# Kernel tuning notes

Measured on AMD Instinct MI355X. Metric: run time of the kernel, lower is better.

## Reference

```python
import jax, jax.numpy as jnp
import numpy as np

NUM_RELATIONS = 4
N_NODES = 20000
N_EDGES = 320000
F_IN = 128
HID = 128
EMB = 128


def _rgcn_conv(x, src, dst, edge_type, edge_weight, W, root, bias):
    """One WeightedRGCNConv layer.
    x: [N, in]; W: [R, in, out]; root: [in, out]; bias: [out].
    Math identical to m = einsum('ei,eio->eo', x[src], W[edge_type]) but computed
    as R grouped matmuls to avoid materializing the [E, in, out] weight copy.
    """
    xj = x[src]  # [E, in] gather
    m = jnp.zeros((xj.shape[0], W.shape[2]), dtype=x.dtype)
    for r in range(W.shape[0]):  # fixed small relation count
        mask = (edge_type == r).astype(x.dtype)[:, None]
        m = m + mask * (xj @ W[r])
    m = m * edge_weight[:, None]
    out = jax.ops.segment_sum(m, dst, num_segments=x.shape[0])  # scatter_add
    return out + x @ root + bias


def setup_inputs() -> dict:
    key = jax.random.key(0)
    ks = jax.random.split(key, 10)
    return {
        "x": jax.random.normal(ks[0], (N_NODES, F_IN), dtype=jnp.float32),
        "edge_index": jax.random.randint(ks[1], (2, N_EDGES), 0, N_NODES, dtype=jnp.int64 if jax.config.jax_enable_x64 else jnp.int32).astype(jnp.int32),
        "edge_type": jax.random.randint(ks[2], (N_EDGES,), 0, NUM_RELATIONS).astype(jnp.int32),
        "edge_weight": jax.random.uniform(ks[3], (N_EDGES,), dtype=jnp.float32),
        "W1": jax.random.normal(ks[4], (NUM_RELATIONS, F_IN, HID), dtype=jnp.float32) * 0.05,
        "root1": jax.random.normal(ks[5], (F_IN, HID), dtype=jnp.float32) * 0.05,
        "b1": jax.random.normal(ks[6], (HID,), dtype=jnp.float32) * 0.05,
        "W2": jax.random.normal(ks[7], (NUM_RELATIONS, HID, EMB), dtype=jnp.float32) * 0.05,
        "root2": jax.random.normal(ks[8], (HID, EMB), dtype=jnp.float32) * 0.05,
        "b2": jax.random.normal(ks[9], (EMB,), dtype=jnp.float32) * 0.05,
    }


def reference(x, edge_index, edge_type, edge_weight, W1, root1, b1, W2, root2, b2):
    src, dst = edge_index[0], edge_index[1]
    # min-max normalize edge weights (as in RGCN.forward)
    ew = (edge_weight - edge_weight.min()) / (edge_weight.max() - edge_weight.min() + 1e-08)
    h = jax.nn.relu(_rgcn_conv(x, src, dst, edge_type, ew, W1, root1, b1))
    h = _rgcn_conv(h, src, dst, edge_type, ew, W2, root2, b2)
    return h
```

## Files before the change

### kernel.cpp

```cpp
#include <hip/hip_runtime.h>

#define NN 20000
#define NE 320000
#define FD 128
#define KTOT 640
#define NSTEP 20

typedef float f32x4 __attribute__((ext_vector_type(4)));
typedef __bf16 bf16x4 __attribute__((ext_vector_type(4)));
typedef __bf16 bf16x8 __attribute__((ext_vector_type(8)));

__device__ __forceinline__ unsigned f2ord(float f) {
  unsigned u = __float_as_uint(f);
  return (u & 0x80000000u) ? ~u : (u | 0x80000000u);
}
__device__ __forceinline__ float ord2f(unsigned u) {
  return (u & 0x80000000u) ? __uint_as_float(u & 0x7FFFFFFFu) : __uint_as_float(~u);
}
__device__ __forceinline__ unsigned pkbf(float a, float b) {
  union { __bf16 h[2]; unsigned u; } p;
  p.h[0] = (__bf16)a; p.h[1] = (__bf16)b; return p.u;
}
__device__ __forceinline__ void gld16(const void* src, void* lds) {
  __builtin_amdgcn_global_load_lds(
      (const unsigned int __attribute__((address_space(1)))*)src,
      (unsigned int __attribute__((address_space(3)))*)lds, 16, 0, 0);
}

__global__ void init_kernel(unsigned* mm, int* deg) {
  int i = blockIdx.x * blockDim.x + threadIdx.x;
  if (i == 0) { mm[0] = 0xFFFFFFFFu; mm[1] = 0u; }
  if (i < NN) deg[i] = 0;
}

__global__ void histmm_kernel(const int* __restrict__ dst, const float* __restrict__ ew,
                              int* deg, unsigned* mm) {
  __shared__ unsigned smn[256], smx[256];
  unsigned lmn = 0xFFFFFFFFu, lmx = 0u;
  for (int i = blockIdx.x * blockDim.x + threadIdx.x; i < NE; i += gridDim.x * blockDim.x) {
    atomicAdd(&deg[dst[i]], 1);
    unsigned o = f2ord(ew[i]);
    lmn = (o < lmn) ? o : lmn;
    lmx = (o > lmx) ? o : lmx;
  }
  smn[threadIdx.x] = lmn; smx[threadIdx.x] = lmx;
  __syncthreads();
  for (int s = 128; s > 0; s >>= 1) {
    if (threadIdx.x < s) {
      unsigned a = smn[threadIdx.x], b = smn[threadIdx.x + s];
      smn[threadIdx.x] = (b < a) ? b : a;
      unsigned c = smx[threadIdx.x], d = smx[threadIdx.x + s];
      smx[threadIdx.x] = (d > c) ? d : c;
    }
    __syncthreads();
  }
  if (threadIdx.x == 0) { atomicMin(&mm[0], smn[0]); atomicMax(&mm[1], smx[0]); }
}

__global__ void scan_kernel(const int* __restrict__ deg, int* offs, int* cursor) {
  __shared__ int part[1024];
  const int CH = (NN + 1023) / 1024;
  int t = threadIdx.x;
  int b = t * CH;
  int e = (b + CH < NN) ? (b + CH) : NN;
  int s = 0;
  for (int i = b; i < e; ++i) s += deg[i];
  part[t] = s;
  __syncthreads();
  for (int off = 1; off < 1024; off <<= 1) {
    int v = part[t];
    int add = (t >= off) ? part[t - off] : 0;
    __syncthreads();
    part[t] = v + add;
    __syncthreads();
  }
  int excl = (t == 0) ? 0 : part[t - 1];
  for (int i = b; i < e; ++i) { offs[i] = excl; cursor[i] = excl; excl += deg[i]; }
  if (t == 1023) offs[NN] = part[1023];
}

__global__ void fill_kernel(const int* __restrict__ src, const int* __restrict__ dst,
                            const int* __restrict__ et, const float* __restrict__ ew,
                            const unsigned* __restrict__ mm, int* cursor,
                            int2* __restrict__ ed) {
  int e = blockIdx.x * blockDim.x + threadIdx.x;
  if (e >= NE) return;
  float mn = ord2f(mm[0]), mx = ord2f(mm[1]);
  float inv = 1.0f / (mx - mn + 1e-8f);
  int d = dst[e];
  int pos = atomicAdd(&cursor[d], 1);
  ed[pos] = make_int2(src[e] | (et[e] << 28), __float_as_int((ew[e] - mn) * inv));
}

__global__ void prep_wt_both(const float* __restrict__ W1, const float* __restrict__ r1,
                             const float* __restrict__ W2, const float* __restrict__ r2,
                             __bf16* __restrict__ wt1, __bf16* __restrict__ wt2) {
  int idx = blockIdx.x * blockDim.x + threadIdx.x;
  if (idx >= 2 * FD * KTOT) return;
  int which = idx / (FD * KTOT);
  int rem = idx % (FD * KTOT);
  int n = rem / KTOT, k = rem % KTOT;
  const float* W = which ? W2 : W1;
  const float* rt = which ? r2 : r1;
  __bf16* wt = which ? wt2 : wt1;
  float v = (k < 512) ? W[(size_t)k * FD + n] : rt[(size_t)(k - 512) * FD + n];
  wt[rem] = (__bf16)v;
}

template <int BF16IN>
__global__ __launch_bounds__(256) void aggregate_kernel(
    const float* __restrict__ xf, const unsigned* __restrict__ xb,
    const int* __restrict__ offs, const int2* __restrict__ ed,
    __bf16* __restrict__ g) {
  int node = (int)((blockIdx.x * blockDim.x + threadIdx.x) >> 6);
  int lane = threadIdx.x & 63;
  if (node >= NN) return;
  int beg = offs[node], end = offs[node + 1];
  float a00 = 0.f, a01 = 0.f, a10 = 0.f, a11 = 0.f;
  float a20 = 0.f, a21 = 0.f, a30 = 0.f, a31 = 0.f;

#define LOADP(E, P0, P1)                                                        \
  do {                                                                          \
    int s_ = (E).x & 0x0FFFFFFF;                                                \
    if (BF16IN) {                                                               \
      unsigned u_ = xb[(size_t)s_ * 64 + lane];                                 \
      P0 = __uint_as_float(u_ << 16);                                           \
      P1 = __uint_as_float(u_ & 0xFFFF0000u);                                   \
    } else {                                                                    \
      float2 v_ = *(const float2*)(xf + (size_t)s_ * FD + lane * 2);            \
      P0 = v_.x; P1 = v_.y;                                                     \
    }                                                                           \
  } while (0)
#define ACCP(E, P0, P1)                                                         \
  do {                                                                          \
    float w_ = __int_as_float((E).y);                                           \
    unsigned r_ = ((unsigned)(E).x) >> 28;                                      \
    float w0_ = (r_ == 0) ? w_ : 0.f, w1_ = (r_ == 1) ? w_ : 0.f;               \
    float w2_ = (r_ == 2) ? w_ : 0.f, w3_ = (r_ == 3) ? w_ : 0.f;               \
    a00 += w0_ * (P0); a01 += w0_ * (P1);                                       \
    a10 += w1_ * (P0); a11 += w1_ * (P1);                                       \
    a20 += w2_ * (P0); a21 += w2_ * (P1);                                       \
    a30 += w3_ * (P0); a31 += w3_ * (P1);                                       \
  } while (0)

  int j = beg;
  for (; j + 4 <= end; j += 4) {
    int2 e0 = ed[j], e1 = ed[j + 1], e2 = ed[j + 2], e3 = ed[j + 3];
    float p00, p01, p10, p11, p20, p21, p30, p31;
    LOADP(e0, p00, p01); LOADP(e1, p10, p11);
    LOADP(e2, p20, p21); LOADP(e3, p30, p31);
    ACCP(e0, p00, p01); ACCP(e1, p10, p11);
    ACCP(e2, p20, p21); ACCP(e3, p30, p31);
  }
  for (; j < end; ++j) {
    int2 e = ed[j];
    float p0, p1;
    LOADP(e, p0, p1);
    ACCP(e, p0, p1);
  }
#undef LOADP
#undef ACCP

  unsigned* g32 = (unsigned*)(g + (size_t)node * KTOT);
  g32[0 * 64 + lane] = pkbf(a00, a01);
  g32[1 * 64 + lane] = pkbf(a10, a11);
  g32[2 * 64 + lane] = pkbf(a20, a21);
  g32[3 * 64 + lane] = pkbf(a30, a31);
  if (BF16IN) {
    g32[4 * 64 + lane] = xb[(size_t)node * 64 + lane];
  } else {
    float2 v = *(const float2*)(xf + (size_t)node * FD + lane * 2);
    g32[4 * 64 + lane] = pkbf(v.x, v.y);
  }
}

template <int OUT_BF16>
__global__ __launch_bounds__(512) void gemm_kernel(
    const __bf16* __restrict__ gA, const __bf16* __restrict__ wt,
    const float* __restrict__ bias, float* __restrict__ outf,
    __bf16* __restrict__ outb) {
  __shared__ __bf16 As[2][64 * 32];
  __shared__ __bf16 Bs[2][128 * 32];
  int tid = threadIdx.x;
  int wave = tid >> 6, lane = tid & 63;
  int wr = wave >> 1, wc = wave & 1;
  int m0 = blockIdx.x * 64;
  int rl = wr * 16 + (lane & 15);
  int kfe = (lane >> 4) * 8;

  unsigned rowpack = 0, colpack[4];
  {
    int arow = tid >> 3, akof = (tid & 7) * 4;
    int bn = tid >> 2, bkof = (tid & 3) * 8;
    bf16x4 v4, one4;
    bf16x8 v8, one8;
#pragma unroll
    for (int i = 0; i < 4; ++i) one4[i] = (__bf16)1.0f;
#pragma unroll
    for (int i = 0; i < 8; ++i) one8[i] = (__bf16)1.0f;
    __bf16 rv = (__bf16)((float)arow * 0.015625f);
#pragma unroll
    for (int i = 0; i < 4; ++i) v4[i] = rv;
    *(bf16x4*)(&As[0][arow * 32 + akof]) = v4;
    *(bf16x8*)(&Bs[0][bn * 32 + bkof]) = one8;
    __syncthreads();
    bf16x8 pa = *(const bf16x8*)(&As[0][rl * 32 + kfe]);
    bf16x8 pb = *(const bf16x8*)(&Bs[0][(wc * 64 + (lane & 15)) * 32 + kfe]);
    f32x4 P1 = __builtin_amdgcn_mfma_f32_16x16x32_bf16(pa, pb, (f32x4){0.f, 0.f, 0.f, 0.f}, 0, 0, 0);
    __syncthreads();
    __bf16 cv = (__bf16)((float)bn * 0.0078125f);
#pragma unroll
    for (int i = 0; i < 8; ++i) v8[i] = cv;
    *(bf16x4*)(&As[0][arow * 32 + akof]) = one4;
    *(bf16x8*)(&Bs[0][bn * 32 + bkof]) = v8;
    __syncthreads();
    bf16x8 pa1 = *(const bf16x8*)(&As[0][rl * 32 + kfe]);
#pragma unroll
    for (int j = 0; j < 4; ++j)
      rowpack |= ((unsigned)(int)(P1[j] * 2.0f + 0.5f)) << (8 * j);
#pragma unroll
    for (int fn = 0; fn < 4; ++fn) {
      bf16x8 pbc = *(const bf16x8*)(&Bs[0][(wc * 64 + fn * 16 + (lane & 15)) * 32 + kfe]);
      f32x4 P2 = __builtin_amdgcn_mfma_f32_16x16x32_bf16(pa1, pbc, (f32x4){0.f, 0.f, 0.f, 0.f}, 0, 0, 0);
      unsigned cp = 0;
#pragma unroll
      for (int j = 0; j < 4; ++j)
        cp |= ((unsigned)(int)(P2[j] * 4.0f + 0.5f)) << (8 * j);
      colpack[fn] = cp;
    }
    __syncthreads();
  }

  f32x4 acc[4];
#pragma unroll
  for (int i = 0; i < 4; ++i) acc[i] = (f32x4){0.f, 0.f, 0.f, 0.f};

  auto stage = [&](int buf, int k0) {
    if (tid < 256) {
      int row = tid >> 2;
      int m = m0 + row;
      if (m >= NN) m = NN - 1;
      gld16(gA + (size_t)m * KTOT + k0 + (tid & 3) * 8, &As[buf][(tid >> 6) * 512]);
    } else {
      int t = tid - 256;
      int wv = t >> 6;
      int r0 = t >> 2;
      gld16(wt + (size_t)r0 * KTOT + k0 + (t & 3) * 8, &Bs[buf][wv * 512]);
      gld16(wt + (size_t)(64 + r0) * KTOT + k0 + (t & 3) * 8, &Bs[buf][2048 + wv * 512]);
    }
  };

  stage(0, 0);
  __syncthreads();
  int cur = 0;
  for (int step = 0; step < NSTEP; ++step) {
    if (step + 1 < NSTEP) stage(cur ^ 1, (step + 1) * 32);
    bf16x8 a = *(const bf16x8*)(&As[cur][rl * 32 + kfe]);
#pragma unroll
    for (int fn = 0; fn < 4; ++fn) {
      bf16x8 b = *(const bf16x8*)(&Bs[cur][(wc * 64 + fn * 16 + (lane & 15)) * 32 + kfe]);
      acc[fn] = __builtin_amdgcn_mfma_f32_16x16x32_bf16(a, b, acc[fn], 0, 0, 0);
    }
    __syncthreads();
    cur ^= 1;
  }

#pragma unroll
  for (int fn = 0; fn < 4; ++fn) {
#pragma unroll
    for (int j = 0; j < 4; ++j) {
      int rloc = (int)((rowpack >> (8 * j)) & 255u);
      int col = (int)((colpack[fn] >> (8 * j)) & 255u);
      int m = m0 + rloc;
      if (m < NN) {
        float v = acc[fn][j] + bias[col];
        if (OUT_BF16) {
          v = fmaxf(v, 0.f);
          outb[(size_t)m * FD + col] = (__bf16)v;
        } else {
          outf[(size_t)m * FD + col] = v;
        }
      }
    }
  }
}

extern "C" void kernel_launch(void* const* d_in, const int* in_sizes, int n_in,
                              void* d_out, int out_size, void* d_ws, size_t ws_size,
                              hipStream_t stream) {
  const float* x  = (const float*)d_in[0];
  const int*   ei = (const int*)d_in[1];
  const int*   et = (const int*)d_in[2];
  const float* ew = (const float*)d_in[3];
  const float* W1 = (const float*)d_in[4];
  const float* r1 = (const float*)d_in[5];
  const float* b1 = (const float*)d_in[6];
  const float* W2 = (const float*)d_in[7];
  const float* r2 = (const float*)d_in[8];
  const float* b2 = (const float*)d_in[9];
  float* out = (float*)d_out;
  const int* src = ei;
  const int* dst = ei + NE;

  char* w = (char*)d_ws;
  size_t o = 0;
  auto take = [&](size_t bytes) -> char* {
    char* p = w + o;
    o += (bytes + 255) & ~(size_t)255;
    return p;
  };
  unsigned* mm  = (unsigned*)take(8);
  int* deg      = (int*)take((size_t)NN * 4);
  int* offs     = (int*)take((size_t)(NN + 1) * 4);
  int* cursor   = (int*)take((size_t)NN * 4);
  int2* ed      = (int2*)take((size_t)NE * 8);
  __bf16* g     = (__bf16*)take((size_t)NN * KTOT * 2);
  __bf16* h1    = (__bf16*)take((size_t)NN * FD * 2);
  __bf16* wt1   = (__bf16*)take((size_t)FD * KTOT * 2);
  __bf16* wt2   = (__bf16*)take((size_t)FD * KTOT * 2);
  (void)ws_size; (void)n_in; (void)in_sizes; (void)out_size;

  hipLaunchKernelGGL(init_kernel, dim3((NN + 255) / 256), dim3(256), 0, stream, mm, deg);
  hipLaunchKernelGGL(histmm_kernel, dim3(512), dim3(256), 0, stream, dst, ew, deg, mm);
  hipLaunchKernelGGL(scan_kernel, dim3(1), dim3(1024), 0, stream, deg, offs, cursor);
  hipLaunchKernelGGL(fill_kernel, dim3((NE + 255) / 256), dim3(256), 0, stream,
                     src, dst, et, ew, mm, cursor, ed);
  hipLaunchKernelGGL(prep_wt_both, dim3((2 * FD * KTOT + 255) / 256), dim3(256), 0, stream,
                     W1, r1, W2, r2, wt1, wt2);
  hipLaunchKernelGGL((aggregate_kernel<0>), dim3(NN / 4), dim3(256), 0, stream,
                     x, (const unsigned*)nullptr, offs, ed, g);
  hipLaunchKernelGGL((gemm_kernel<1>), dim3((NN + 63) / 64), dim3(512), 0, stream,
                     g, wt1, b1, (float*)nullptr, h1);
  hipLaunchKernelGGL((aggregate_kernel<1>), dim3(NN / 4), dim3(256), 0, stream,
                     (const float*)nullptr, (const unsigned*)h1, offs, ed, g);
  hipLaunchKernelGGL((gemm_kernel<0>), dim3((NN + 63) / 64), dim3(512), 0, stream,
                     g, wt2, b2, out, (__bf16*)nullptr);
}
```

Before: 168.7 us.

## Fuse edge aggregation with GEMM per node tile through LDS

Replaces the separate aggregate and GEMM kernels with one fused kernel per layer. Each block aggregates 32 nodes into a swizzled LDS tile and then multiplies that tile by the bf16 weights, with B fragments read straight from global memory. This removes the round trip of the 640-wide g buffer through global memory and two kernel launches. Layer-1 input x is now converted to bf16 up front in init_kernel, which lowers the precision of the first gather. The cost is less parallelism for the gather, since each wave serially handles 4 nodes, and no LDS staging or reuse of the weights.

```diff
diff --git a/kernel.cpp b/kernel.cpp
--- a/kernel.cpp
+++ b/kernel.cpp
@@ -4,10 +4,9 @@
 #define NE 320000
 #define FD 128
 #define KTOT 640
-#define NSTEP 20
+#define BM 32
 
 typedef float f32x4 __attribute__((ext_vector_type(4)));
-typedef __bf16 bf16x4 __attribute__((ext_vector_type(4)));
 typedef __bf16 bf16x8 __attribute__((ext_vector_type(8)));
 
 __device__ __forceinline__ unsigned f2ord(float f) {
@@ -21,16 +20,19 @@
   union { __bf16 h[2]; unsigned u; } p;
   p.h[0] = (__bf16)a; p.h[1] = (__bf16)b; return p.u;
 }
-__device__ __forceinline__ void gld16(const void* src, void* lds) {
-  __builtin_amdgcn_global_load_lds(
-      (const unsigned int __attribute__((address_space(1)))*)src,
-      (unsigned int __attribute__((address_space(3)))*)lds, 16, 0, 0);
-}
-
-__global__ void init_kernel(unsigned* mm, int* deg) {
+
+__global__ void init_kernel(unsigned* mm, int* deg,
+                            const float* __restrict__ x, unsigned* __restrict__ xb) {
   int i = blockIdx.x * blockDim.x + threadIdx.x;
   if (i == 0) { mm[0] = 0xFFFFFFFFu; mm[1] = 0u; }
   if (i < NN) deg[i] = 0;
+  if (i < NN * FD / 4) {
+    float4 v = *(const float4*)(x + (size_t)i * 4);
+    uint2 p;
+    p.x = pkbf(v.x, v.y);
+    p.y = pkbf(v.z, v.w);
+    *(uint2*)(xb + (size_t)i * 2) = p;
+  }
 }
 
 __global__ void histmm_kernel(const int* __restrict__ dst, const float* __restrict__ ew,
@@ -107,180 +109,137 @@
   wt[rem] = (__bf16)v;
 }
 
-template <int BF16IN>
-__global__ __launch_bounds__(256) void aggregate_kernel(
-    const float* __restrict__ xf, const unsigned* __restrict__ xb,
+template <int BF16OUT>
+__global__ __launch_bounds__(512, 2) void fused_kernel(
+    const unsigned* __restrict__ xb,
     const int* __restrict__ offs, const int2* __restrict__ ed,
-    __bf16* __restrict__ g) {
-  int node = (int)((blockIdx.x * blockDim.x + threadIdx.x) >> 6);
-  int lane = threadIdx.x & 63;
-  if (node >= NN) return;
-  int beg = offs[node], end = offs[node + 1];
-  float a00 = 0.f, a01 = 0.f, a10 = 0.f, a11 = 0.f;
-  float a20 = 0.f, a21 = 0.f, a30 = 0.f, a31 = 0.f;
-
-#define LOADP(E, P0, P1)                                                        \
-  do {                                                                          \
-    int s_ = (E).x & 0x0FFFFFFF;                                                \
-    if (BF16IN) {                                                               \
-      unsigned u_ = xb[(size_t)s_ * 64 + lane];                                 \
-      P0 = __uint_as_float(u_ << 16);                                           \
-      P1 = __uint_as_float(u_ & 0xFFFF0000u);                                   \
-    } else {                                                                    \
-      float2 v_ = *(const float2*)(xf + (size_t)s_ * FD + lane * 2);            \
-      P0 = v_.x; P1 = v_.y;                                                     \
-    }                                                                           \
+    const __bf16* __restrict__ wt, const float* __restrict__ bias,
+    float* __restrict__ outf, __bf16* __restrict__ outb) {
+  __shared__ unsigned As32[BM * 320];
+  int tid = threadIdx.x;
+  int wave = tid >> 6, lane = tid & 63;
+  int wr = wave >> 2, wc = wave & 3;
+  int m0 = blockIdx.x * BM;
+  int rl = wr * 16 + (lane & 15);
+  int kfe = (lane >> 4) * 8;
+  int c0 = wc * 32 + (lane & 15);
+  const f32x4 zz = {0.f, 0.f, 0.f, 0.f};
+
+  unsigned rowpack = 0, colpack0 = 0, colpack1 = 0;
+  {
+    if (tid < 256) {
+      int row = tid >> 3;
+      int wl = (tid & 7) * 2;
+      unsigned val = pkbf((float)row * 0.03125f, (float)row * 0.03125f);
+      int sw2 = (row & 7) << 2;
+      As32[row * 320 + (wl ^ sw2)] = val;
+      As32[row * 320 + ((wl + 1) ^ sw2)] = val;
+    }
+    __syncthreads();
+    const char* Arow = (const char*)As32 + rl * 1280;
+    int swb = (rl & 7) << 4;
+    bf16x8 pa = *(const bf16x8*)(Arow + ((kfe * 2) ^ swb));
+    bf16x8 ones, bp0, bp1;
+#pragma unroll
+    for (int i = 0; i < 8; ++i) ones[i] = (__bf16)1.0f;
+    __bf16 c0v = (__bf16)((float)c0 * 0.0078125f);
+    __bf16 c1v = (__bf16)((float)(c0 + 16) * 0.0078125f);
+#pragma unroll
+    for (int i = 0; i < 8; ++i) { bp0[i] = c0v; bp1[i] = c1v; }
+    f32x4 P1 = __builtin_amdgcn_mfma_f32_16x16x32_bf16(pa, ones, zz, 0, 0, 0);
+    f32x4 P2a = __builtin_amdgcn_mfma_f32_16x16x32_bf16(ones, bp0, zz, 0, 0, 0);
+    f32x4 P2b = __builtin_amdgcn_mfma_f32_16x16x32_bf16(ones, bp1, zz, 0, 0, 0);
+#pragma unroll
+    for (int j = 0; j < 4; ++j) {
+      rowpack |= ((unsigned)(int)(P1[j] + 0.5f)) << (8 * j);
+      colpack0 |= ((unsigned)(int)(P2a[j] * 4.0f + 0.5f)) << (8 * j);
+      colpack1 |= ((unsigned)(int)(P2b[j] * 4.0f + 0.5f)) << (8 * j);
+    }
+    __syncthreads();
+  }
+
+#define LOADP(E, P0, P1)                                                \
+  do {                                                                  \
+    int s_ = (E).x & 0x0FFFFFFF;                                        \
+    unsigned u_ = xb[(size_t)s_ * 64 + lane];                           \
+    P0 = __uint_as_float(u_ << 16);                                     \
+    P1 = __uint_as_float(u_ & 0xFFFF0000u);                             \
   } while (0)
-#define ACCP(E, P0, P1)                                                         \
-  do {                                                                          \
-    float w_ = __int_as_float((E).y);                                           \
-    unsigned r_ = ((unsigned)(E).x) >> 28;                                      \
-    float w0_ = (r_ == 0) ? w_ : 0.f, w1_ = (r_ == 1) ? w_ : 0.f;               \
-    float w2_ = (r_ == 2) ? w_ : 0.f, w3_ = (r_ == 3) ? w_ : 0.f;               \
-    a00 += w0_ * (P0); a01 += w0_ * (P1);                                       \
-    a10 += w1_ * (P0); a11 += w1_ * (P1);                                       \
-    a20 += w2_ * (P0); a21 += w2_ * (P1);                                       \
-    a30 += w3_ * (P0); a31 += w3_ * (P1);                                       \
+#define ACCP(E, P0, P1)                                                 \
+  do {                                                                  \
+    float w_ = __int_as_float((E).y);                                   \
+    unsigned r_ = ((unsigned)(E).x) >> 28;                              \
+    float w0_ = (r_ == 0) ? w_ : 0.f, w1_ = (r_ == 1) ? w_ : 0.f;       \
+    float w2_ = (r_ == 2) ? w_ : 0.f, w3_ = (r_ == 3) ? w_ : 0.f;       \
+    a00 += w0_ * (P0); a01 += w0_ * (P1);                               \
+    a10 += w1_ * (P0); a11 += w1_ * (P1);                               \
+    a20 += w2_ * (P0); a21 += w2_ * (P1);                               \
+    a30 += w3_ * (P0); a31 += w3_ * (P1);                               \
   } while (0)
 
-  int j = beg;
-  for (; j + 4 <= end; j += 4) {
-    int2 e0 = ed[j], e1 = ed[j + 1], e2 = ed[j + 2], e3 = ed[j + 3];
-    float p00, p01, p10, p11, p20, p21, p30, p31;
-    LOADP(e0, p00, p01); LOADP(e1, p10, p11);
-    LOADP(e2, p20, p21); LOADP(e3, p30, p31);
-    ACCP(e0, p00, p01); ACCP(e1, p10, p11);
-    ACCP(e2, p20, p21); ACCP(e3, p30, p31);
-  }
-  for (; j < end; ++j) {
-    int2 e = ed[j];
-    float p0, p1;
-    LOADP(e, p0, p1);
-    ACCP(e, p0, p1);
+  for (int nl = 0; nl < 4; ++nl) {
+    int nloc = (wave << 2) + nl;
+    int node = m0 + nloc;
+    int beg = offs[node], end = offs[node + 1];
+    float a00 = 0.f, a01 = 0.f, a10 = 0.f, a11 = 0.f;
+    float a20 = 0.f, a21 = 0.f, a30 = 0.f, a31 = 0.f;
+    int j = beg;
+    for (; j + 4 <= end; j += 4) {
+      int2 e0 = ed[j], e1 = ed[j + 1], e2 = ed[j + 2], e3 = ed[j + 3];
+      float p00, p01, p10, p11, p20, p21, p30, p31;
+      LOADP(e0, p00, p01); LOADP(e1, p10, p11);
+      LOADP(e2, p20, p21); LOADP(e3, p30, p31);
+      ACCP(e0, p00, p01); ACCP(e1, p10, p11);
+      ACCP(e2, p20, p21); ACCP(e3, p30, p31);
+    }
+    for (; j < end; ++j) {
+      int2 e = ed[j];
+      float p0, p1;
+      LOADP(e, p0, p1);
+      ACCP(e, p0, p1);
+    }
+    int sw2 = (nloc & 7) << 2;
+    unsigned* row = As32 + nloc * 320;
+    row[(0 * 64 + lane) ^ sw2] = pkbf(a00, a01);
+    row[(1 * 64 + lane) ^ sw2] = pkbf(a10, a11);
+    row[(2 * 64 + lane) ^ sw2] = pkbf(a20, a21);
+    row[(3 * 64 + lane) ^ sw2] = pkbf(a30, a31);
+    row[(4 * 64 + lane) ^ sw2] = xb[(size_t)node * 64 + lane];
   }
 #undef LOADP
 #undef ACCP
-
-  unsigned* g32 = (unsigned*)(g + (size_t)node * KTOT);
-  g32[0 * 64 + lane] = pkbf(a00, a01);
-  g32[1 * 64 + lane] = pkbf(a10, a11);
-  g32[2 * 64 + lane] = pkbf(a20, a21);
-  g32[3 * 64 + lane] = pkbf(a30, a31);
-  if (BF16IN) {
-    g32[4 * 64 + lane] = xb[(size_t)node * 64 + lane];
-  } else {
-    float2 v = *(const float2*)(xf + (size_t)node * FD + lane * 2);
-    g32[4 * 64 + lane] = pkbf(v.x, v.y);
-  }
-}
-
-template <int OUT_BF16>
-__global__ __launch_bounds__(512) void gemm_kernel(
-    const __bf16* __restrict__ gA, const __bf16* __restrict__ wt,
-    const float* __restrict__ bias, float* __restrict__ outf,
-    __bf16* __restrict__ outb) {
-  __shared__ __bf16 As[2][64 * 32];
-  __shared__ __bf16 Bs[2][128 * 32];
-  int tid = threadIdx.x;
-  int wave = tid >> 6, lane = tid & 63;
-  int wr = wave >> 1, wc = wave & 1;
-  int m0 = blockIdx.x * 64;
-  int rl = wr * 16 + (lane & 15);
-  int kfe = (lane >> 4) * 8;
-
-  unsigned rowpack = 0, colpack[4];
-  {
-    int arow = tid >> 3, akof = (tid & 7) * 4;
-    int bn = tid >> 2, bkof = (tid & 3) * 8;
-    bf16x4 v4, one4;
-    bf16x8 v8, one8;
-#pragma unroll
-    for (int i = 0; i < 4; ++i) one4[i] = (__bf16)1.0f;
-#pragma unroll
-    for (int i = 0; i < 8; ++i) one8[i] = (__bf16)1.0f;
-    __bf16 rv = (__bf16)((float)arow * 0.015625f);
-#pragma unroll
-    for (int i = 0; i < 4; ++i) v4[i] = rv;
-    *(bf16x4*)(&As[0][arow * 32 + akof]) = v4;
-    *(bf16x8*)(&Bs[0][bn * 32 + bkof]) = one8;
-    __syncthreads();
-    bf16x8 pa = *(const bf16x8*)(&As[0][rl * 32 + kfe]);
-    bf16x8 pb = *(const bf16x8*)(&Bs[0][(wc * 64 + (lane & 15)) * 32 + kfe]);
-    f32x4 P1 = __builtin_amdgcn_mfma_f32_16x16x32_bf16(pa, pb, (f32x4){0.f, 0.f, 0.f, 0.f}, 0, 0, 0);
-    __syncthreads();
-    __bf16 cv = (__bf16)((float)bn * 0.0078125f);
-#pragma unroll
-    for (int i = 0; i < 8; ++i) v8[i] = cv;
-    *(bf16x4*)(&As[0][arow * 32 + akof]) = one4;
-    *(bf16x8*)(&Bs[0][bn * 32 + bkof]) = v8;
-    __syncthreads();
-    bf16x8 pa1 = *(const bf16x8*)(&As[0][rl * 32 + kfe]);
-#pragma unroll
-    for (int j = 0; j < 4; ++j)
-      rowpack |= ((unsigned)(int)(P1[j] * 2.0f + 0.5f)) << (8 * j);
-#pragma unroll
-    for (int fn = 0; fn < 4; ++fn) {
-      bf16x8 pbc = *(const bf16x8*)(&Bs[0][(wc * 64 + fn * 16 + (lane & 15)) * 32 + kfe]);
-      f32x4 P2 = __builtin_amdgcn_mfma_f32_16x16x32_bf16(pa1, pbc, (f32x4){0.f, 0.f, 0.f, 0.f}, 0, 0, 0);
-      unsigned cp = 0;
-#pragma unroll
-      for (int j = 0; j < 4; ++j)
-        cp |= ((unsigned)(int)(P2[j] * 4.0f + 0.5f)) << (8 * j);
-      colpack[fn] = cp;
-    }
-    __syncthreads();
-  }
-
-  f32x4 acc[4];
-#pragma unroll
-  for (int i = 0; i < 4; ++i) acc[i] = (f32x4){0.f, 0.f, 0.f, 0.f};
-
-  auto stage = [&](int buf, int k0) {
-    if (tid < 256) {
-      int row = tid >> 2;
-      int m = m0 + row;
-      if (m >= NN) m = NN - 1;
-      gld16(gA + (size_t)m * KTOT + k0 + (tid & 3) * 8, &As[buf][(tid >> 6) * 512]);
-    } else {
-      int t = tid - 256;
-      int wv = t >> 6;
-      int r0 = t >> 2;
-      gld16(wt + (size_t)r0 * KTOT + k0 + (t & 3) * 8, &Bs[buf][wv * 512]);
-      gld16(wt + (size_t)(64 + r0) * KTOT + k0 + (t & 3) * 8, &Bs[buf][2048 + wv * 512]);
-    }
-  };
-
-  stage(0, 0);
   __syncthreads();
-  int cur = 0;
-  for (int step = 0; step < NSTEP; ++step) {
-    if (step + 1 < NSTEP) stage(cur ^ 1, (step + 1) * 32);
-    bf16x8 a = *(const bf16x8*)(&As[cur][rl * 32 + kfe]);
-#pragma unroll
-    for (int fn = 0; fn < 4; ++fn) {
-      bf16x8 b = *(const bf16x8*)(&Bs[cur][(wc * 64 + fn * 16 + (lane & 15)) * 32 + kfe]);
-      acc[fn] = __builtin_amdgcn_mfma_f32_16x16x32_bf16(a, b, acc[fn], 0, 0, 0);
-    }
-    __syncthreads();
-    cur ^= 1;
-  }
-
-#pragma unroll
-  for (int fn = 0; fn < 4; ++fn) {
-#pragma unroll
-    for (int j = 0; j < 4; ++j) {
-      int rloc = (int)((rowpack >> (8 * j)) & 255u);
-      int col = (int)((colpack[fn] >> (8 * j)) & 255u);
-      int m = m0 + rloc;
-      if (m < NN) {
-        float v = acc[fn][j] + bias[col];
-        if (OUT_BF16) {
-          v = fmaxf(v, 0.f);
-          outb[(size_t)m * FD + col] = (__bf16)v;
-        } else {
-          outf[(size_t)m * FD + col] = v;
-        }
-      }
+
+  f32x4 acc0 = zz, acc1 = zz;
+  const __bf16* w0p = wt + (size_t)c0 * KTOT + kfe;
+  const __bf16* w1p = w0p + 16 * KTOT;
+  const char* Arow = (const char*)As32 + rl * 1280;
+  int swb = (rl & 7) << 4;
+#pragma unroll
+  for (int step = 0; step < 20; ++step) {
+    int b = (step * 64 + kfe * 2) ^ swb;
+    bf16x8 a = *(const bf16x8*)(Arow + b);
+    bf16x8 b0 = *(const bf16x8*)(w0p + step * 32);
+    bf16x8 b1 = *(const bf16x8*)(w1p + step * 32);
+    acc0 = __builtin_amdgcn_mfma_f32_16x16x32_bf16(a, b0, acc0, 0, 0, 0);
+    acc1 = __builtin_amdgcn_mfma_f32_16x16x32_bf16(a, b1, acc1, 0, 0, 0);
+  }
+
+#pragma unroll
+  for (int j = 0; j < 4; ++j) {
+    int rloc = (int)((rowpack >> (8 * j)) & 255u);
+    size_t m = (size_t)(m0 + rloc);
+    {
+      int col = (int)((colpack0 >> (8 * j)) & 255u);
+      float v = acc0[j] + bias[col];
+      if (BF16OUT) outb[m * FD + col] = (__bf16)fmaxf(v, 0.f);
+      else outf[m * FD + col] = v;
+    }
+    {
+      int col = (int)((colpack1 >> (8 * j)) & 255u);
+      float v = acc1[j] + bias[col];
+      if (BF16OUT) outb[m * FD + col] = (__bf16)fmaxf(v, 0.f);
+      else outf[m * FD + col] = v;
     }
   }
 }
@@ -314,25 +273,22 @@
   int* offs     = (int*)take((size_t)(NN + 1) * 4);
   int* cursor   = (int*)take((size_t)NN * 4);
   int2* ed      = (int2*)take((size_t)NE * 8);
-  __bf16* g     = (__bf16*)take((size_t)NN * KTOT * 2);
+  unsigned* xb  = (unsigned*)take((size_t)NN * 64 * 4);
   __bf16* h1    = (__bf16*)take((size_t)NN * FD * 2);
   __bf16* wt1   = (__bf16*)take((size_t)FD * KTOT * 2);
   __bf16* wt2   = (__bf16*)take((size_t)FD * KTOT * 2);
   (void)ws_size; (void)n_in; (void)in_sizes; (void)out_size;
 
-  hipLaunchKernelGGL(init_kernel, dim3((NN + 255) / 256), dim3(256), 0, stream, mm, deg);
+  hipLaunchKernelGGL(init_kernel, dim3((NN * FD / 4 + 255) / 256), dim3(256), 0, stream,
+                     mm, deg, x, xb);
   hipLaunchKernelGGL(histmm_kernel, dim3(512), dim3(256), 0, stream, dst, ew, deg, mm);
   hipLaunchKernelGGL(scan_kernel, dim3(1), dim3(1024), 0, stream, deg, offs, cursor);
   hipLaunchKernelGGL(fill_kernel, dim3((NE + 255) / 256), dim3(256), 0, stream,
                      src, dst, et, ew, mm, cursor, ed);
   hipLaunchKernelGGL(prep_wt_both, dim3((2 * FD * KTOT + 255) / 256), dim3(256), 0, stream,
                      W1, r1, W2, r2, wt1, wt2);
-  hipLaunchKernelGGL((aggregate_kernel<0>), dim3(NN / 4), dim3(256), 0, stream,
-                     x, (const unsigned*)nullptr, offs, ed, g);
-  hipLaunchKernelGGL((gemm_kernel<1>), dim3((NN + 63) / 64), dim3(512), 0, stream,
-                     g, wt1, b1, (float*)nullptr, h1);
-  hipLaunchKernelGGL((aggregate_kernel<1>), dim3(NN / 4), dim3(256), 0, stream,
-                     (const float*)nullptr, (const unsigned*)h1, offs, ed, g);
-  hipLaunchKernelGGL((gemm_kernel<0>), dim3((NN + 63) / 64), dim3(512), 0, stream,
-                     g, wt2, b2, out, (__bf16*)nullptr);
-}
+  hipLaunchKernelGGL((fused_kernel<1>), dim3(NN / BM), dim3(512), 0, stream,
+                     xb, offs, ed, wt1, b1, (float*)nullptr, h1);
+  hipLaunchKernelGGL((fused_kernel<0>), dim3(NN / BM), dim3(512), 0, stream,
+                     (const unsigned*)h1, offs, ed, wt2, b2, out, (__bf16*)nullptr);
+}
```

Result: slower. 192.5 us (+14.1%).

## Pre-convert x to bf16, merge prep kernels, add L2 warm-up loads

Applied to the files above, without the earlier changes.

Converts input features x to bf16 in a merged prep kernel that also zeroes degree counters and transposes weights, so both aggregation passes gather half-width bf16 rows instead of fp32. The fill kernel additionally loads the bf16 x buffer to pull it into cache before the first aggregation. A new warm kernel streams h1 before the second aggregation for the same purpose. The warm-up passes cost extra bandwidth and a launch, and they only pay off if the data stays resident in cache until the following kernel runs.

```diff
diff --git a/kernel.cpp b/kernel.cpp
--- a/kernel.cpp
+++ b/kernel.cpp
@@ -27,10 +27,30 @@
       (unsigned int __attribute__((address_space(3)))*)lds, 16, 0, 0);
 }
 
-__global__ void init_kernel(unsigned* mm, int* deg) {
+__global__ void prep_kernel(unsigned* mm, int* deg,
+                            const float* __restrict__ x, unsigned* __restrict__ xb,
+                            const float* __restrict__ W1, const float* __restrict__ r1,
+                            const float* __restrict__ W2, const float* __restrict__ r2,
+                            __bf16* __restrict__ wt1, __bf16* __restrict__ wt2) {
   int i = blockIdx.x * blockDim.x + threadIdx.x;
   if (i == 0) { mm[0] = 0xFFFFFFFFu; mm[1] = 0u; }
   if (i < NN) deg[i] = 0;
+  if (i < 2 * FD * KTOT) {
+    int which = i / (FD * KTOT);
+    int rem = i % (FD * KTOT);
+    int n = rem / KTOT, k = rem % KTOT;
+    const float* W = which ? W2 : W1;
+    const float* rt = which ? r2 : r1;
+    float v = (k < 512) ? W[(size_t)k * FD + n] : rt[(size_t)(k - 512) * FD + n];
+    (which ? wt2 : wt1)[rem] = (__bf16)v;
+  }
+  if (i < NN * FD / 4) {
+    float4 v = *(const float4*)(x + (size_t)i * 4);
+    uint2 p;
+    p.x = pkbf(v.x, v.y);
+    p.y = pkbf(v.z, v.w);
+    *(uint2*)(xb + (size_t)i * 2) = p;
+  }
 }
 
 __global__ void histmm_kernel(const int* __restrict__ dst, const float* __restrict__ ew,
@@ -82,7 +102,7 @@
 __global__ void fill_kernel(const int* __restrict__ src, const int* __restrict__ dst,
                             const int* __restrict__ et, const float* __restrict__ ew,
                             const unsigned* __restrict__ mm, int* cursor,
-                            int2* __restrict__ ed) {
+                            int2* __restrict__ ed, const uint4* __restrict__ xb4) {
   int e = blockIdx.x * blockDim.x + threadIdx.x;
   if (e >= NE) return;
   float mn = ord2f(mm[0]), mx = ord2f(mm[1]);
@@ -90,26 +110,20 @@
   int d = dst[e];
   int pos = atomicAdd(&cursor[d], 1);
   ed[pos] = make_int2(src[e] | (et[e] << 28), __float_as_int((ew[e] - mn) * inv));
-}
-
-__global__ void prep_wt_both(const float* __restrict__ W1, const float* __restrict__ r1,
-                             const float* __restrict__ W2, const float* __restrict__ r2,
-                             __bf16* __restrict__ wt1, __bf16* __restrict__ wt2) {
-  int idx = blockIdx.x * blockDim.x + threadIdx.x;
-  if (idx >= 2 * FD * KTOT) return;
-  int which = idx / (FD * KTOT);
-  int rem = idx % (FD * KTOT);
-  int n = rem / KTOT, k = rem % KTOT;
-  const float* W = which ? W2 : W1;
-  const float* rt = which ? r2 : r1;
-  __bf16* wt = which ? wt2 : wt1;
-  float v = (k < 512) ? W[(size_t)k * FD + n] : rt[(size_t)(k - 512) * FD + n];
-  wt[rem] = (__bf16)v;
-}
-
-template <int BF16IN>
+  uint4 wv = xb4[e];
+  asm volatile("" :: "v"(wv.x), "v"(wv.y), "v"(wv.z), "v"(wv.w));
+}
+
+__global__ void warm_kernel(const uint4* __restrict__ p, int n4) {
+  int i = blockIdx.x * blockDim.x + threadIdx.x;
+  if (i < n4) {
+    uint4 v = p[i];
+    asm volatile("" :: "v"(v.x), "v"(v.y), "v"(v.z), "v"(v.w));
+  }
+}
+
 __global__ __launch_bounds__(256) void aggregate_kernel(
-    const float* __restrict__ xf, const unsigned* __restrict__ xb,
+    const unsigned* __restrict__ xb,
     const int* __restrict__ offs, const int2* __restrict__ ed,
     __bf16* __restrict__ g) {
   int node = (int)((blockIdx.x * blockDim.x + threadIdx.x) >> 6);
@@ -119,28 +133,25 @@
   float a00 = 0.f, a01 = 0.f, a10 = 0.f, a11 = 0.f;
   float a20 = 0.f, a21 = 0.f, a30 = 0.f, a31 = 0.f;
 
-#define LOADP(E, P0, P1)                                                        \
-  do {                                                                          \
-    int s_ = (E).x & 0x0FFFFFFF;                                                \
-    if (BF16IN) {                                                               \
-      unsigned u_ = xb[(size_t)s_ * 64 + lane];                                 \
-      P0 = __uint_as_float(u_ << 16);                                           \
-      P1 = __uint_as_float(u_ & 0xFFFF0000u);                                   \
-    } else {                                                                    \
-      float2 v_ = *(const float2*)(xf + (size_t)s_ * FD + lane * 2);            \
-      P0 = v_.x; P1 = v_.y;                                                     \
-    }                                                                           \
+#define LOADP(E, P0, P1)                                                \
+  do {                                                                  \
+    int zs_ = (E).x & 0x0FFFFFFF;                                       \
+    unsigned zu_ = xb[(size_t)zs_ * 64 + lane];                         \
+    P0 = __uint_as_float(zu_ << 16);                                    \
+    P1 = __uint_as_float(zu_ & 0xFFFF0000u);                            \
   } while (0)
-#define ACCP(E, P0, P1)                                                         \
-  do {                                                                          \
-    float w_ = __int_as_float((E).y);                                           \
-    unsigned r_ = ((unsigned)(E).x) >> 28;                                      \
-    float w0_ = (r_ == 0) ? w_ : 0.f, w1_ = (r_ == 1) ? w_ : 0.f;               \
-    float w2_ = (r_ == 2) ? w_ : 0.f, w3_ = (r_ == 3) ? w_ : 0.f;               \
-    a00 += w0_ * (P0); a01 += w0_ * (P1);                                       \
-    a10 += w1_ * (P0); a11 += w1_ * (P1);                                       \
-    a20 += w2_ * (P0); a21 += w2_ * (P1);                                       \
-    a30 += w3_ * (P0); a31 += w3_ * (P1);                                       \
+#define ACCP(E, P0, P1)                                                 \
+  do {                                                                  \
+    float zw_ = __int_as_float((E).y);                                  \
+    unsigned zr_ = ((unsigned)(E).x) >> 28;                             \
+    float zw0_ = (zr_ == 0) ? zw_ : 0.f;                                \
+    float zw1_ = (zr_ == 1) ? zw_ : 0.f;                                \
+    float zw2_ = (zr_ == 2) ? zw_ : 0.f;                                \
+    float zw3_ = (zr_ == 3) ? zw_ : 0.f;                                \
+    a00 += zw0_ * (P0); a01 += zw0_ * (P1);                             \
+    a10 += zw1_ * (P0); a11 += zw1_ * (P1);                             \
+    a20 += zw2_ * (P0); a21 += zw2_ * (P1);                             \
+    a30 += zw3_ * (P0); a31 += zw3_ * (P1);                             \
   } while (0)
 
   int j = beg;
@@ -166,12 +177,7 @@
   g32[1 * 64 + lane] = pkbf(a10, a11);
   g32[2 * 64 + lane] = pkbf(a20, a21);
   g32[3 * 64 + lane] = pkbf(a30, a31);
-  if (BF16IN) {
-    g32[4 * 64 + lane] = xb[(size_t)node * 64 + lane];
-  } else {
-    float2 v = *(const float2*)(xf + (size_t)node * FD + lane * 2);
-    g32[4 * 64 + lane] = pkbf(v.x, v.y);
-  }
+  g32[4 * 64 + lane] = xb[(size_t)node * 64 + lane];
 }
 
 template <int OUT_BF16>
@@ -313,26 +319,27 @@
   int* deg      = (int*)take((size_t)NN * 4);
   int* offs     = (int*)take((size_t)(NN + 1) * 4);
   int* cursor   = (int*)take((size_t)NN * 4);
-  int2* ed      = (int2*)take((size_t)NE * 8);
+  int2* ed      = (int2*)take((size_t)(NE + 8) * 8);
+  unsigned* xb  = (unsigned*)take((size_t)NN * 64 * 4);
   __bf16* g     = (__bf16*)take((size_t)NN * KTOT * 2);
   __bf16* h1    = (__bf16*)take((size_t)NN * FD * 2);
   __bf16* wt1   = (__bf16*)take((size_t)FD * KTOT * 2);
   __bf16* wt2   = (__bf16*)take((size_t)FD * KTOT * 2);
   (void)ws_size; (void)n_in; (void)in_sizes; (void)out_size;
 
-  hipLaunchKernelGGL(init_kernel, dim3((NN + 255) / 256), dim3(256), 0, stream, mm, deg);
+  hipLaunchKernelGGL(prep_kernel, dim3((NN * FD / 4 + 255) / 256), dim3(256), 0, stream,
+                     mm, deg, x, xb, W1, r1, W2, r2, wt1, wt2);
   hipLaunchKernelGGL(histmm_kernel, dim3(512), dim3(256), 0, stream, dst, ew, deg, mm);
   hipLaunchKernelGGL(scan_kernel, dim3(1), dim3(1024), 0, stream, deg, offs, cursor);
   hipLaunchKernelGGL(fill_kernel, dim3((NE + 255) / 256), dim3(256), 0, stream,
-                     src, dst, et, ew, mm, cursor, ed);
-  hipLaunchKernelGGL(prep_wt_both, dim3((2 * FD * KTOT + 255) / 256), dim3(256), 0, stream,
-                     W1, r1, W2, r2, wt1, wt2);
-  hipLaunchKernelGGL((aggregate_kernel<0>), dim3(NN / 4), dim3(256), 0, stream,
-                     x, (const unsigned*)nullptr, offs, ed, g);
+                     src, dst, et, ew, mm, cursor, ed, (const uint4*)xb);
+  hipLaunchKernelGGL(aggregate_kernel, dim3(NN / 4), dim3(256), 0, stream, xb, offs, ed, g);
   hipLaunchKernelGGL((gemm_kernel<1>), dim3((NN + 63) / 64), dim3(512), 0, stream,
                      g, wt1, b1, (float*)nullptr, h1);
-  hipLaunchKernelGGL((aggregate_kernel<1>), dim3(NN / 4), dim3(256), 0, stream,
-                     (const float*)nullptr, (const unsigned*)h1, offs, ed, g);
+  hipLaunchKernelGGL(warm_kernel, dim3((NN * 64 / 4 + 255) / 256), dim3(256), 0, stream,
+                     (const uint4*)h1, NN * 64 / 4);
+  hipLaunchKernelGGL(aggregate_kernel, dim3(NN / 4), dim3(256), 0, stream,
+                     (const unsigned*)h1, offs, ed, g);
   hipLaunchKernelGGL((gemm_kernel<0>), dim3((NN + 63) / 64), dim3(512), 0, stream,
                      g, wt2, b2, out, (__bf16*)nullptr);
 }
```

After: 162.7 us. 3.5% less time.
